# Optimization experiments

Hardware: AMD Instinct MI355X
Metric: run time of the kernel (lower is better)

Reference implementation:

```python
import jax, jax.numpy as jnp
import numpy as np
from jax import lax


def _c1x1(t, w, b=None):
    # t: [B,C,H,W], w: [O,C] (1x1 conv == channel matmul)
    y = jnp.einsum('bchw,oc->bohw', t, w)
    if b is not None:
        y = y + b[None, :, None, None]
    return y


def _mamba(u, in_w, conv_w, conv_b, xproj_w, dt_w, dt_b, A_log, Dp, out_w):
    # u: [B,L,d_model]; Mamba block (mamba_ssm defaults: in/out/x_proj bias=False)
    B, L, _ = u.shape
    d_inner = conv_w.shape[0]
    d_state = A_log.shape[1]
    dt_rank = dt_w.shape[1]
    d_conv = conv_w.shape[2]
    xz = jnp.einsum('bld,ed->ble', u, in_w)          # [B,L,2*d_inner]
    xc, z = xz[..., :d_inner], xz[..., d_inner:]
    # depthwise causal conv1d over seq
    xt = jnp.pad(xc.transpose(0, 2, 1), ((0, 0), (0, 0), (d_conv - 1, 0)))
    xt = lax.conv_general_dilated(xt, conv_w, (1,), 'VALID',
                                  feature_group_count=d_inner,
                                  dimension_numbers=('NCH', 'OIH', 'NCH'))
    xc = jax.nn.silu(xt + conv_b[None, :, None]).transpose(0, 2, 1)  # [B,L,d_inner]
    dbc = jnp.einsum('bld,ed->ble', xc, xproj_w)     # [B,L,dt_rank+2*d_state]
    dt = dbc[..., :dt_rank]
    B_ = dbc[..., dt_rank:dt_rank + d_state]
    C_ = dbc[..., dt_rank + d_state:]
    delta = jax.nn.softplus(jnp.einsum('blr,dr->bld', dt, dt_w) + dt_b)  # [B,L,d_inner]
    A = -jnp.exp(A_log)                              # [d_inner,d_state]
    dA = jnp.exp(delta[..., None] * A)               # [B,L,D,N]
    dBu = delta[..., None] * B_[:, :, None, :] * xc[..., None]
    def step(h, inp):
        dA_t, dBu_t, c_t = inp
        h = dA_t * h + dBu_t                         # [B,D,N]
        y = jnp.einsum('bdn,bn->bd', h, c_t)
        return h, y
    h0 = jnp.zeros((B, d_inner, d_state), dtype=u.dtype)
    _, ys = lax.scan(step, h0, (dA.transpose(1, 0, 2, 3),
                                dBu.transpose(1, 0, 2, 3),
                                C_.transpose(1, 0, 2)))
    y = ys.transpose(1, 0, 2) + xc * Dp              # [B,L,d_inner]
    y = y * jax.nn.silu(z)
    return jnp.einsum('bld,od->blo', y, out_w)       # [B,L,d_model]


def setup_inputs() -> dict:
    key = jax.random.key(0)
    B, C, H, W = 8, 128, 160, 160
    mip, d_in, d_st, d_r, d_cv = 8, 256, 16, 8, 4
    ks = iter(jax.random.split(key, 64))
    def rn(shape, s=0.05):
        return (jax.random.normal(next(ks), shape, dtype=jnp.float32) * s)
    inp = {'x': jax.random.normal(next(ks), (B, C, H, W), dtype=jnp.float32)}
    inp.update(conv1_w=rn((mip, C)), conv1_b=rn((mip,)),
               bn_g=jnp.ones((mip,)), bn_b=jnp.zeros((mip,)),
               bn_m=jnp.zeros((mip,)), bn_v=jnp.ones((mip,)),
               convh_w=rn((C, mip)), convh_b=rn((C,)),
               convw_w=rn((C, mip)), convw_b=rn((C,)),
               mlpx_w1=rn((C, C)), mlpx_b1=rn((C,)), mlpx_w2=rn((C, C)), mlpx_b2=rn((C,)),
               mlpy_w1=rn((C, C)), mlpy_b1=rn((C,)), mlpy_w2=rn((C, C)), mlpy_b2=rn((C,)),
               adjust_w=rn((C, 2 * C)))
    for p in ('mx', 'my'):
        inp[p + '_in_w'] = rn((2 * d_in, C))
        inp[p + '_conv_w'] = rn((d_in, 1, d_cv), 0.3)
        inp[p + '_conv_b'] = rn((d_in,))
        inp[p + '_xproj_w'] = rn((d_r + 2 * d_st, d_in))
        inp[p + '_dt_w'] = rn((d_in, d_r))
        inp[p + '_dt_b'] = rn((d_in,))
        inp[p + '_Alog'] = jnp.log(jnp.broadcast_to(jnp.arange(1, d_st + 1, dtype=jnp.float32), (d_in, d_st)))
        inp[p + '_D'] = jnp.ones((d_in,))
        inp[p + '_out_w'] = rn((C, d_in))
    return inp


def reference(x, conv1_w, conv1_b, bn_g, bn_b, bn_m, bn_v, convh_w, convh_b,
              convw_w, convw_b, mlpx_w1, mlpx_b1, mlpx_w2, mlpx_b2,
              mlpy_w1, mlpy_b1, mlpy_w2, mlpy_b2, adjust_w,
              mx_in_w, mx_conv_w, mx_conv_b, mx_xproj_w, mx_dt_w, mx_dt_b,
              mx_Alog, mx_D, mx_out_w,
              my_in_w, my_conv_w, my_conv_b, my_xproj_w, my_dt_w, my_dt_b,
              my_Alog, my_D, my_out_w):
    B, C, H, W = x.shape
    gelu = lambda t: jax.nn.gelu(t, approximate=False)
    # CoordAttWithMLP
    x_h = x.mean(3, keepdims=True)                      # [B,C,H,1]
    x_w = x.mean(2, keepdims=True).transpose(0, 1, 3, 2)  # [B,C,W,1]
    y = jnp.concatenate([x_h, x_w], axis=2)             # [B,C,H+W,1]
    y = _c1x1(y, conv1_w, conv1_b)
    y = (y - bn_m[None, :, None, None]) * jax.lax.rsqrt(bn_v + 1e-5)[None, :, None, None]
    y = y * bn_g[None, :, None, None] + bn_b[None, :, None, None]
    y = gelu(y)
    a_h = _c1x1(y[:, :, :H], convh_w, convh_b)          # [B,C,H,1] (pre-sigmoid)
    a_w = _c1x1(y[:, :, H:].transpose(0, 1, 3, 2), convw_w, convw_b)  # [B,C,1,W]
    # EfficientMambaAttention00
    ux = x.mean(3).transpose(0, 2, 1)                   # [B,H,C]
    x_x = _mamba(ux, mx_in_w, mx_conv_w, mx_conv_b, mx_xproj_w,
                 mx_dt_w, mx_dt_b, mx_Alog, mx_D, mx_out_w)
    x_x = x_x.transpose(0, 2, 1)[..., None]             # [B,C,H,1]
    x_x = jax.nn.sigmoid(x_x + a_h)
    x_x = _c1x1(gelu(_c1x1(x_x, mlpx_w1, mlpx_b1)), mlpx_w2, mlpx_b2)
    uy = x.mean(2).transpose(0, 2, 1)                   # [B,W,C]
    x_y = _mamba(uy, my_in_w, my_conv_w, my_conv_b, my_xproj_w,
                 my_dt_w, my_dt_b, my_Alog, my_D, my_out_w)
    x_y = x_y.transpose(0, 2, 1)[:, :, None, :]         # [B,C,1,W]
    x_y = jax.nn.sigmoid(x_y + a_w)
    x_y = _c1x1(gelu(_c1x1(x_y, mlpy_w1, mlpy_b1)), mlpy_w2, mlpy_b2)
    # combine
    result_h = jax.nn.sigmoid(a_h) * x_y                # [B,C,H,W]
    result_w = jax.nn.sigmoid(a_w) * x_x                # [B,C,H,W]
    out1 = _c1x1(jnp.concatenate([result_h, result_w], axis=1), adjust_w)
    return x * out1
```

## Files before the change

kernel.cpp:

```cpp
#include <hip/hip_runtime.h>
#include <hip/hip_bf16.h>
#include <math.h>


typedef __attribute__((ext_vector_type(8))) short short8;
typedef __attribute__((ext_vector_type(4))) float f32x4;

__device__ __forceinline__ float sigm_(float x){ return 1.f/(1.f+__expf(-x)); }
__device__ __forceinline__ float silu_(float x){ return x/(1.f+__expf(-x)); }
__device__ __forceinline__ float gelu_(float x){ return 0.5f*x*(1.f+erff(x*0.7071067811865476f)); }
__device__ __forceinline__ float softplus_(float x){ return (x>20.f)?x:log1pf(__expf(x)); }

__global__ void k_means(const float* __restrict__ x, float* __restrict__ xh, float* __restrict__ xw){
  int bc = blockIdx.x;
  const float* xt = x + (size_t)bc*25600;
  int tid = threadIdx.x, wave = tid>>6, lane = tid&63;
  __shared__ float4 colpart[4][40];
  float csx=0.f, csy=0.f, csz=0.f, csw=0.f;
  for (int i=0;i<40;i++){
    int h = wave*40+i;
    float4 v = make_float4(0.f,0.f,0.f,0.f);
    if (lane<40) v = ((const float4*)(xt + h*160))[lane];
    csx+=v.x; csy+=v.y; csz+=v.z; csw+=v.w;
    float r = v.x+v.y+v.z+v.w;
    for (int off=32; off>0; off>>=1) r += __shfl_down(r, off, 64);
    if (lane==0) xh[(size_t)bc*160+h] = r*(1.f/160.f);
  }
  if (lane<40) colpart[wave][lane] = make_float4(csx,csy,csz,csw);
  __syncthreads();
  if (tid<40){
    float4 a=colpart[0][tid], b=colpart[1][tid], c=colpart[2][tid], d=colpart[3][tid];
    float4 s = make_float4((a.x+b.x+c.x+d.x)*(1.f/160.f), (a.y+b.y+c.y+d.y)*(1.f/160.f),
                           (a.z+b.z+c.z+d.z)*(1.f/160.f), (a.w+b.w+c.w+d.w)*(1.f/160.f));
    ((float4*)(xw + (size_t)bc*160))[tid] = s;
  }
}

__global__ void k_ybranch(const float* __restrict__ xh, const float* __restrict__ xw,
                          const float* __restrict__ w1, const float* __restrict__ b1,
                          const float* __restrict__ bg, const float* __restrict__ bb,
                          const float* __restrict__ bm, const float* __restrict__ bv,
                          float* __restrict__ ybuf){
  int gid = blockIdx.x*blockDim.x + threadIdx.x;
  if (gid >= 8*320) return;
  int b = gid/320, p = gid%320;
  const float* in = (p<160) ? (xh + (size_t)b*128*160 + p) : (xw + (size_t)b*128*160 + (p-160));
  float acc[8] = {0,0,0,0,0,0,0,0};
  for (int c=0;c<128;c++){
    float u = in[c*160];
    #pragma unroll
    for (int m=0;m<8;m++) acc[m] += w1[m*128+c]*u;
  }
  #pragma unroll
  for (int m=0;m<8;m++){
    float val = acc[m] + b1[m];
    val = (val - bm[m]) * rsqrtf(bv[m] + 1e-5f);
    val = val * bg[m] + bb[m];
    ybuf[(b*320+p)*8+m] = gelu_(val);
  }
}

__global__ void k_ahw(const float* __restrict__ ybuf,
                      const float* __restrict__ wh, const float* __restrict__ bh,
                      const float* __restrict__ ww, const float* __restrict__ bw,
                      float* __restrict__ a_h, float* __restrict__ a_w,
                      float* __restrict__ SH, float* __restrict__ SW){
  int gid = blockIdx.x*blockDim.x + threadIdx.x;
  if (gid >= 8*128*320) return;
  int p = gid%320; int c = (gid/320)%128; int b = gid/(320*128);
  const float* yv = ybuf + (size_t)(b*320+p)*8;
  const float* w = (p<160)? (wh + c*8) : (ww + c*8);
  float acc = (p<160)? bh[c] : bw[c];
  #pragma unroll
  for (int m=0;m<8;m++) acc += w[m]*yv[m];
  if (p<160){
    size_t o = ((size_t)(b*128+c))*160+p;
    a_h[o] = acc; SH[o] = sigm_(acc);
  } else {
    size_t o = ((size_t)(b*128+c))*160+(p-160);
    a_w[o] = acc; SW[o] = sigm_(acc);
  }
}

__global__ __launch_bounds__(256) void k_inproj(
                         const float* __restrict__ xh, const float* __restrict__ xw,
                         const float* __restrict__ inw0, const float* __restrict__ inw1,
                         float* __restrict__ xcpre, float* __restrict__ zb){
  __shared__ float uS[8][128];
  int blk = blockIdx.x;
  int g = blk/160, rem = blk%160, b = rem/20, lt = rem%20, lbase = lt*8;
  int t = threadIdx.x;
  const float* src = (g==0)? xh : xw;
  {
    int c = t>>1, lh = t&1;
    float4 v = *(const float4*)(src + ((size_t)(b*128+c))*160 + lbase + lh*4);
    uS[lh*4+0][c]=v.x; uS[lh*4+1][c]=v.y; uS[lh*4+2][c]=v.z; uS[lh*4+3][c]=v.w;
  }
  __syncthreads();
  const float* inw = (g==0)? inw0 : inw1;
  const float* w0p = inw + (size_t)t*128;
  const float* w1p = inw + (size_t)(t+256)*128;
  float acc0[8]={0,0,0,0,0,0,0,0}, acc1[8]={0,0,0,0,0,0,0,0};
  for (int ct=0; ct<16; ct++){
    float4 wa = *(const float4*)(w0p + ct*8);
    float4 wb = *(const float4*)(w0p + ct*8 + 4);
    float4 wc = *(const float4*)(w1p + ct*8);
    float4 wd = *(const float4*)(w1p + ct*8 + 4);
    #pragma unroll
    for (int l=0;l<8;l++){
      float4 ua = *(const float4*)&uS[l][ct*8];
      float4 ub = *(const float4*)&uS[l][ct*8+4];
      acc0[l] += wa.x*ua.x + wa.y*ua.y + wa.z*ua.z + wa.w*ua.w
               + wb.x*ub.x + wb.y*ub.y + wb.z*ub.z + wb.w*ub.w;
      acc1[l] += wc.x*ua.x + wc.y*ua.y + wc.z*ua.z + wc.w*ua.w
               + wd.x*ub.x + wd.y*ub.y + wd.z*ub.z + wd.w*ub.w;
    }
  }
  size_t ob = ((size_t)(g*8+b)*160 + lbase)*256;
  #pragma unroll
  for (int l=0;l<8;l++){
    xcpre[ob + (size_t)l*256 + t] = acc0[l];
    zb   [ob + (size_t)l*256 + t] = acc1[l];
  }
}

__global__ void k_conv(const float* __restrict__ xcpre,
                       const float* __restrict__ cw0, const float* __restrict__ cb0,
                       const float* __restrict__ cw1, const float* __restrict__ cb1,
                       float* __restrict__ xcb){
  int gid = blockIdx.x*blockDim.x + threadIdx.x;
  if (gid >= 2*8*160*256) return;
  int d = gid & 255; int t = gid >> 8; int l = t % 160; int gb = t / 160; int g = gb >> 3;
  const float* cw = ((g==0)? cw0 : cw1) + d*4;
  float acc = ((g==0)? cb0 : cb1)[d];
  const float* base = xcpre + (size_t)gb*160*256 + d;
  #pragma unroll
  for (int k=0;k<4;k++){
    int ls = l-3+k;
    if (ls>=0) acc += cw[k] * base[(size_t)ls*256];
  }
  xcb[gid] = silu_(acc);
}

__global__ void k_prep(const float* __restrict__ adjw, __hip_bfloat16* __restrict__ adjwb){
  int i = blockIdx.x*256 + threadIdx.x;
  if (i < 32768) adjwb[i] = __float2bfloat16(adjw[i]);
}

__global__ __launch_bounds__(256) void k_xproj(
                        const float* __restrict__ xcb,
                        const float* __restrict__ xp0, const float* __restrict__ xp1,
                        float* __restrict__ dbc){
  __shared__ float xv[32][260];
  int blk = blockIdx.x;
  int g = blk/40, rem = blk%40, b = rem/5, lt = rem%5, lbase = lt*32;
  int t = threadIdx.x;
  size_t base = ((size_t)(g*8+b)*160 + lbase)*256;
  for (int i=t; i<8192; i+=256){ int l=i>>8, d=i&255; xv[l][d] = xcb[base+i]; }
  __syncthreads();
  int l = t>>3, s = t&7;
  const float* xp = (g==0)? xp0 : xp1;
  size_t orow = ((size_t)(g*8+b)*160 + lbase + l)*40;
  for (int q=0;q<5;q++){
    int j = s + q*8;
    const float* w = xp + j*256;
    float acc=0.f;
    for (int dd=0; dd<256; dd+=8){
      float4 wa = *(const float4*)(w+dd);
      float4 wb = *(const float4*)(w+dd+4);
      float4 ua = *(const float4*)&xv[l][dd];
      float4 ub = *(const float4*)&xv[l][dd+4];
      acc += wa.x*ua.x + wa.y*ua.y + wa.z*ua.z + wa.w*ua.w
           + wb.x*ub.x + wb.y*ub.y + wb.z*ub.z + wb.w*ub.w;
    }
    dbc[orow + j] = acc;
  }
}

__global__ __launch_bounds__(256) void k_scan(
                       const float* __restrict__ dbc,
                       const float* __restrict__ xcb, const float* __restrict__ zb,
                       const float* __restrict__ dtw0, const float* __restrict__ dtb0,
                       const float* __restrict__ dtw1, const float* __restrict__ dtb1,
                       const float* __restrict__ Alog0, const float* __restrict__ Alog1,
                       const float* __restrict__ D0, const float* __restrict__ D1,
                       float* __restrict__ ysb){
  __shared__ float dsS[160][16];
  __shared__ float BS [160][16];
  __shared__ float CS [160][16];
  __shared__ float xcS[160][16];
  __shared__ float yS [160][16];
  int blk = blockIdx.x;
  int gb = blk >> 4, dblk = blk & 15, g = gb >> 3;
  int dbase = dblk*16;
  int t = threadIdx.x;
  size_t base = (size_t)gb*160*256;
  const float* db = dbc + (size_t)gb*6400;
  const float* dtwG = (g==0)? dtw0 : dtw1;
  const float* dtbG = (g==0)? dtb0 : dtb1;

  #pragma unroll
  for (int i=0;i<10;i++){
    int item = t + 256*i;
    int l = item>>4, c = item&15;
    const float* r = db + l*40;
    int d = dbase + c;
    const float* wt = dtwG + d*8;
    float4 w0 = *(const float4*)wt;
    float4 w1 = *(const float4*)(wt+4);
    float4 r0 = *(const float4*)r;
    float4 r1 = *(const float4*)(r+4);
    float dt = dtbG[d] + w0.x*r0.x+w0.y*r0.y+w0.z*r0.z+w0.w*r0.w
                       + w1.x*r1.x+w1.y*r1.y+w1.z*r1.z+w1.w*r1.w;
    dsS[l][c] = softplus_(dt);
    BS [l][c] = r[8+c];
    CS [l][c] = r[24+c];
    xcS[l][c] = xcb[base + (size_t)l*256 + dbase + c];
  }
  __syncthreads();

  int dloc = t>>4, n = t&15;
  int d = dbase + dloc;
  float A  = -__expf(((g==0)? Alog0 : Alog1)[d*16+n]);
  float Dd = ((g==0)? D0 : D1)[d];
  float h = 0.f;
  for (int lc=0; lc<160; lc+=8){
    float ds8[8], B8[8], C8[8], xc8[8];
    #pragma unroll
    for (int j=0;j<8;j++){
      ds8[j]=dsS[lc+j][dloc]; B8[j]=BS[lc+j][n];
      C8[j]=CS[lc+j][n];      xc8[j]=xcS[lc+j][dloc];
    }
    #pragma unroll
    for (int j=0;j<8;j++){
      float dA = __expf(ds8[j]*A);
      h = dA*h + ds8[j]*B8[j]*xc8[j];
      float p = h*C8[j];
      p += __shfl_xor(p,1,16); p += __shfl_xor(p,2,16);
      p += __shfl_xor(p,4,16); p += __shfl_xor(p,8,16);
      if (n==0) yS[lc+j][dloc] = p + xc8[j]*Dd;
    }
  }
  __syncthreads();

  #pragma unroll
  for (int i=0;i<10;i++){
    int item = t + 256*i;
    int l = item>>4, c = item&15;
    size_t gi = base + (size_t)l*256 + dbase + c;
    ysb[gi] = yS[l][c] * silu_(zb[gi]);
  }
}

__global__ __launch_bounds__(256) void k_post(
                       const float* __restrict__ ysb,
                       const float* __restrict__ ow0, const float* __restrict__ ow1,
                       const float* __restrict__ a_h, const float* __restrict__ a_w,
                       const float* __restrict__ w1x, const float* __restrict__ b1x,
                       const float* __restrict__ w1y, const float* __restrict__ b1y,
                       const float* __restrict__ w2x, const float* __restrict__ b2x,
                       const float* __restrict__ w2y, const float* __restrict__ b2y,
                       float* __restrict__ Qx, float* __restrict__ Qy){
  __shared__ float ysS[10][256];
  __shared__ float Sc[10][128];
  __shared__ float Sp[10][128];
  int blk = blockIdx.x;
  int g = blk>>7, rem = blk&127, b = rem>>4, lt = rem&15, lbase = lt*10;
  int t = threadIdx.x; int c = t&127, kh = t>>7;
  size_t ybase = ((size_t)(g*8+b)*160 + lbase)*256;
  for (int i=t; i<2560; i+=256) ((float*)ysS)[i] = ysb[ybase+i];
  __syncthreads();
  float acc[10];
  {
    const float* w = ((g==0)? ow0 : ow1) + (size_t)c*256 + kh*128;
    #pragma unroll
    for (int l=0;l<10;l++) acc[l]=0.f;
    for (int ct=0; ct<16; ct++){
      float4 wa = *(const float4*)(w + ct*8);
      float4 wb = *(const float4*)(w + ct*8 + 4);
      #pragma unroll
      for (int l=0;l<10;l++){
        float4 ua = *(const float4*)&ysS[l][kh*128+ct*8];
        float4 ub = *(const float4*)&ysS[l][kh*128+ct*8+4];
        acc[l] += wa.x*ua.x + wa.y*ua.y + wa.z*ua.z + wa.w*ua.w
                + wb.x*ub.x + wb.y*ub.y + wb.z*ub.z + wb.w*ub.w;
      }
    }
  }
  if (kh==1){ for (int l=0;l<10;l++) Sc[l][c] = acc[l]; }
  __syncthreads();
  if (kh==0){
    const float* a = ((g==0)? a_h : a_w) + ((size_t)(b*128+c))*160 + lbase;
    #pragma unroll
    for (int l=0;l<10;l++) Sp[l][c] = sigm_(acc[l] + Sc[l][c] + a[l]);
  }
  __syncthreads();
  {
    const float* w = ((g==0)? w1x : w1y) + (size_t)c*128 + kh*64;
    #pragma unroll
    for (int l=0;l<10;l++) acc[l]=0.f;
    for (int ct=0; ct<8; ct++){
      float4 wa = *(const float4*)(w + ct*8);
      float4 wb = *(const float4*)(w + ct*8 + 4);
      #pragma unroll
      for (int l=0;l<10;l++){
        float4 ua = *(const float4*)&Sp[l][kh*64+ct*8];
        float4 ub = *(const float4*)&Sp[l][kh*64+ct*8+4];
        acc[l] += wa.x*ua.x + wa.y*ua.y + wa.z*ua.z + wa.w*ua.w
                + wb.x*ub.x + wb.y*ub.y + wb.z*ub.z + wb.w*ub.w;
      }
    }
  }
  if (kh==1){ for (int l=0;l<10;l++) Sc[l][c] = acc[l]; }
  __syncthreads();
  if (kh==0){
    float bb = ((g==0)? b1x : b1y)[c];
    float tv[10];
    #pragma unroll
    for (int l=0;l<10;l++) tv[l] = gelu_(bb + acc[l] + Sc[l][c]);
    __syncthreads();
    #pragma unroll
    for (int l=0;l<10;l++) Sp[l][c] = tv[l];
  } else {
    __syncthreads();
  }
  __syncthreads();
  {
    const float* w = ((g==0)? w2x : w2y) + (size_t)c*128 + kh*64;
    #pragma unroll
    for (int l=0;l<10;l++) acc[l]=0.f;
    for (int ct=0; ct<8; ct++){
      float4 wa = *(const float4*)(w + ct*8);
      float4 wb = *(const float4*)(w + ct*8 + 4);
      #pragma unroll
      for (int l=0;l<10;l++){
        float4 ua = *(const float4*)&Sp[l][kh*64+ct*8];
        float4 ub = *(const float4*)&Sp[l][kh*64+ct*8+4];
        acc[l] += wa.x*ua.x + wa.y*ua.y + wa.z*ua.z + wa.w*ua.w
                + wb.x*ub.x + wb.y*ub.y + wb.z*ub.z + wb.w*ub.w;
      }
    }
  }
  if (kh==1){ for (int l=0;l<10;l++) Sc[l][c] = acc[l]; }
  __syncthreads();
  if (kh==0){
    float bb = ((g==0)? b2x : b2y)[c];
    float* Q = (g==0)? Qx : Qy;
    size_t orow = ((size_t)(b*128+c))*160 + lbase;
    #pragma unroll
    for (int l=0;l<10;l++) Q[orow + l] = bb + acc[l] + Sc[l][c];
  }
}

__global__ __launch_bounds__(256) void k_final_mfma(
                       const float* __restrict__ x,
                       const float* __restrict__ SH, const float* __restrict__ SW,
                       const float* __restrict__ Qx, const float* __restrict__ Qy,
                       const __hip_bfloat16* __restrict__ adjwb, float* __restrict__ out){
  __shared__ __hip_bfloat16 F[80*136];
  int blk = blockIdx.x;
  int b = blk/320; int rem = blk%320; int h = rem>>1; int wh = rem&1;
  int wbase = wh*80;
  int tid = threadIdx.x;
  int kq = tid & 127, whh = tid >> 7;
  int wid = tid>>6, lane = tid&63, quad = lane>>4, l16 = lane&15;

  f32x4 acc[2][5];
  #pragma unroll
  for (int i=0;i<2;i++)
    #pragma unroll
    for (int nt=0;nt<5;nt++) acc[i][nt] = (f32x4){0.f,0.f,0.f,0.f};

  #pragma unroll
  for (int ch=0; ch<2; ch++){
    {
      size_t rowoff = ((size_t)(b*128+kq))*160;
      float s;
      const float* rp;
      if (ch==0){ s = SH[rowoff + h]; rp = Qy + rowoff + wbase + whh*40; }
      else      { s = Qx[rowoff + h]; rp = SW + rowoff + wbase + whh*40; }
      const float4* rp4 = (const float4*)rp;
      #pragma unroll
      for (int u=0; u<10; u++){
        float4 v = rp4[u];
        int wr = whh*40 + u*4;
        F[(wr+0)*136 + kq] = __float2bfloat16(s*v.x);
        F[(wr+1)*136 + kq] = __float2bfloat16(s*v.y);
        F[(wr+2)*136 + kq] = __float2bfloat16(s*v.z);
        F[(wr+3)*136 + kq] = __float2bfloat16(s*v.w);
      }
    }
    __syncthreads();
    short8 bfrag[2][4];
    #pragma unroll
    for (int i=0;i<2;i++){
      const __hip_bfloat16* bp = adjwb + (size_t)((wid*2+i)*16 + l16)*256 + ch*128 + quad*8;
      #pragma unroll
      for (int kc=0;kc<4;kc++) bfrag[i][kc] = *(const short8*)(bp + kc*32);
    }
    #pragma unroll
    for (int nt=0; nt<5; nt++){
      const __hip_bfloat16* ap = &F[(nt*16 + l16)*136 + quad*8];
      #pragma unroll
      for (int kc=0;kc<4;kc++){
        short8 af = *(const short8*)(ap + kc*32);
        acc[0][nt] = __builtin_amdgcn_mfma_f32_16x16x32_bf16(af, bfrag[0][kc], acc[0][nt], 0,0,0);
        acc[1][nt] = __builtin_amdgcn_mfma_f32_16x16x32_bf16(af, bfrag[1][kc], acc[1][nt], 0,0,0);
      }
    }
    if (ch==0) __syncthreads();
  }
  #pragma unroll
  for (int i=0;i<2;i++){
    int o = (wid*2+i)*16 + l16;
    size_t rowb = (((size_t)(b*128+o))*160 + h)*160;
    #pragma unroll
    for (int nt=0; nt<5; nt++){
      int w0 = wbase + nt*16 + quad*4;
      float4 xv = *(const float4*)(x + rowb + w0);
      f32x4 a = acc[i][nt];
      float4 ov = make_float4(xv.x*a[0], xv.y*a[1], xv.z*a[2], xv.w*a[3]);
      *(float4*)(out + rowb + w0) = ov;
    }
  }
}

extern "C" void kernel_launch(void* const* d_in, const int* in_sizes, int n_in,
                              void* d_out, int out_size, void* d_ws, size_t ws_size,
                              hipStream_t stream) {
  #define W(i) ((const float*)d_in[i])
  const float* X = W(0);
  float* ws = (float*)d_ws;
  float* xh    = ws;
  float* xw    = xh    + 163840;
  float* ybuf  = xw    + 163840;
  float* ah    = ybuf  + 20480;
  float* aw    = ah    + 163840;
  float* xcpre = aw    + 163840;
  float* zb    = xcpre + 655360;
  float* xcb   = zb    + 655360;
  float* dbc   = xcb   + 655360;
  float* ysb   = dbc   + 102400;
  float* Qx    = ysb   + 655360;
  float* Qy    = Qx    + 163840;
  __hip_bfloat16* adjwb = (__hip_bfloat16*)xcpre;
  float* SH    = xcpre + 16384;
  float* SW    = SH    + 163840;

  k_means  <<<1024, 256, 0, stream>>>(X, xh, xw);
  k_ybranch<<<10,   256, 0, stream>>>(xh, xw, W(1), W(2), W(3), W(4), W(5), W(6), ybuf);
  k_inproj <<<320,  256, 0, stream>>>(xh, xw, W(20), W(29), xcpre, zb);
  k_conv   <<<2560, 256, 0, stream>>>(xcpre, W(21), W(22), W(30), W(31), xcb);
  k_prep   <<<128,  256, 0, stream>>>(W(19), adjwb);
  k_ahw    <<<1280, 256, 0, stream>>>(ybuf, W(7), W(8), W(9), W(10), ah, aw, SH, SW);
  k_xproj  <<<80,   256, 0, stream>>>(xcb, W(23), W(32), dbc);
  k_scan   <<<256,  256, 0, stream>>>(dbc, xcb, zb, W(24), W(25), W(33), W(34),
                                      W(26), W(35), W(27), W(36), ysb);
  k_post   <<<256,  256, 0, stream>>>(ysb, W(28), W(37), ah, aw,
                                      W(11), W(12), W(15), W(16),
                                      W(13), W(14), W(17), W(18), Qx, Qy);
  k_final_mfma<<<2560, 256, 0, stream>>>(X, SH, SW, Qx, Qy, adjwb, (float*)d_out);
  #undef W
}
```

Baseline: 466.9 us.

## Transpose SH/Qx layouts, prefetch loads, remap blocks and use nontemporal stores in final kernel

SH and Qx are now written transposed ([b,h,c]), so the per-channel scalar loads in the final kernel become coalesced across kq. The final kernel issues all Qy/SW row loads and the x tile loads early, so they overlap the first MFMA phase. The block index is swizzled across batches, and output stores use nontemporal hints to avoid cache pollution. Costs: more registers held live and uncoalesced transposed writes in k_ahw and k_post.

```diff
diff --git a/kernel.cpp b/kernel.cpp
--- a/kernel.cpp
+++ b/kernel.cpp
@@ -64,7 +64,7 @@
                       const float* __restrict__ wh, const float* __restrict__ bh,
                       const float* __restrict__ ww, const float* __restrict__ bw,
                       float* __restrict__ a_h, float* __restrict__ a_w,
-                      float* __restrict__ SH, float* __restrict__ SW){
+                      float* __restrict__ SHT, float* __restrict__ SW){
   int gid = blockIdx.x*blockDim.x + threadIdx.x;
   if (gid >= 8*128*320) return;
   int p = gid%320; int c = (gid/320)%128; int b = gid/(320*128);
@@ -75,7 +75,8 @@
   for (int m=0;m<8;m++) acc += w[m]*yv[m];
   if (p<160){
     size_t o = ((size_t)(b*128+c))*160+p;
-    a_h[o] = acc; SH[o] = sigm_(acc);
+    a_h[o] = acc;
+    SHT[((size_t)(b*160+p))*128 + c] = sigm_(acc);
   } else {
     size_t o = ((size_t)(b*128+c))*160+(p-160);
     a_w[o] = acc; SW[o] = sigm_(acc);
@@ -260,7 +261,7 @@
                        const float* __restrict__ w1y, const float* __restrict__ b1y,
                        const float* __restrict__ w2x, const float* __restrict__ b2x,
                        const float* __restrict__ w2y, const float* __restrict__ b2y,
-                       float* __restrict__ Qx, float* __restrict__ Qy){
+                       float* __restrict__ QxT, float* __restrict__ Qy){
   __shared__ float ysS[10][256];
   __shared__ float Sc[10][128];
   __shared__ float Sp[10][128];
@@ -345,56 +346,65 @@
   __syncthreads();
   if (kh==0){
     float bb = ((g==0)? b2x : b2y)[c];
-    float* Q = (g==0)? Qx : Qy;
-    size_t orow = ((size_t)(b*128+c))*160 + lbase;
-    #pragma unroll
-    for (int l=0;l<10;l++) Q[orow + l] = bb + acc[l] + Sc[l][c];
+    if (g==0){
+      #pragma unroll
+      for (int l=0;l<10;l++)
+        QxT[((size_t)(b*160 + lbase + l))*128 + c] = bb + acc[l] + Sc[l][c];
+    } else {
+      size_t orow = ((size_t)(b*128+c))*160 + lbase;
+      #pragma unroll
+      for (int l=0;l<10;l++) Qy[orow + l] = bb + acc[l] + Sc[l][c];
+    }
   }
 }
 
 __global__ __launch_bounds__(256) void k_final_mfma(
                        const float* __restrict__ x,
-                       const float* __restrict__ SH, const float* __restrict__ SW,
-                       const float* __restrict__ Qx, const float* __restrict__ Qy,
+                       const float* __restrict__ SHT, const float* __restrict__ SW,
+                       const float* __restrict__ QxT, const float* __restrict__ Qy,
                        const __hip_bfloat16* __restrict__ adjwb, float* __restrict__ out){
   __shared__ __hip_bfloat16 F[80*136];
-  int blk = blockIdx.x;
+  int blk0 = blockIdx.x;
+  int blk = (blk0 & 7)*320 + (blk0 >> 3);
   int b = blk/320; int rem = blk%320; int h = rem>>1; int wh = rem&1;
   int wbase = wh*80;
   int tid = threadIdx.x;
   int kq = tid & 127, whh = tid >> 7;
   int wid = tid>>6, lane = tid&63, quad = lane>>4, l16 = lane&15;
 
+  float s0 = SHT[((size_t)(b*160+h))*128 + kq];
+  float s1 = QxT[((size_t)(b*160+h))*128 + kq];
+
+  size_t prow = ((size_t)(b*128+kq))*160 + wbase + whh*40;
+  const float4* rp0 = (const float4*)(Qy + prow);
+  const float4* rp1 = (const float4*)(SW + prow);
+
+  float4 v0[10], v1[10];
+  #pragma unroll
+  for (int u=0;u<10;u++) v0[u] = rp0[u];
+  #pragma unroll
+  for (int u=0;u<10;u++) v1[u] = rp1[u];
+  #pragma unroll
+  for (int u=0;u<10;u++){
+    int wr = whh*40 + u*4;
+    F[(wr+0)*136 + kq] = __float2bfloat16(s0*v0[u].x);
+    F[(wr+1)*136 + kq] = __float2bfloat16(s0*v0[u].y);
+    F[(wr+2)*136 + kq] = __float2bfloat16(s0*v0[u].z);
+    F[(wr+3)*136 + kq] = __float2bfloat16(s0*v0[u].w);
+  }
+  __syncthreads();
+
   f32x4 acc[2][5];
   #pragma unroll
   for (int i=0;i<2;i++)
     #pragma unroll
     for (int nt=0;nt<5;nt++) acc[i][nt] = (f32x4){0.f,0.f,0.f,0.f};
 
-  #pragma unroll
-  for (int ch=0; ch<2; ch++){
-    {
-      size_t rowoff = ((size_t)(b*128+kq))*160;
-      float s;
-      const float* rp;
-      if (ch==0){ s = SH[rowoff + h]; rp = Qy + rowoff + wbase + whh*40; }
-      else      { s = Qx[rowoff + h]; rp = SW + rowoff + wbase + whh*40; }
-      const float4* rp4 = (const float4*)rp;
-      #pragma unroll
-      for (int u=0; u<10; u++){
-        float4 v = rp4[u];
-        int wr = whh*40 + u*4;
-        F[(wr+0)*136 + kq] = __float2bfloat16(s*v.x);
-        F[(wr+1)*136 + kq] = __float2bfloat16(s*v.y);
-        F[(wr+2)*136 + kq] = __float2bfloat16(s*v.z);
-        F[(wr+3)*136 + kq] = __float2bfloat16(s*v.w);
-      }
-    }
-    __syncthreads();
+  {
     short8 bfrag[2][4];
     #pragma unroll
     for (int i=0;i<2;i++){
-      const __hip_bfloat16* bp = adjwb + (size_t)((wid*2+i)*16 + l16)*256 + ch*128 + quad*8;
+      const __hip_bfloat16* bp = adjwb + (size_t)((wid*2+i)*16 + l16)*256 + quad*8;
       #pragma unroll
       for (int kc=0;kc<4;kc++) bfrag[i][kc] = *(const short8*)(bp + kc*32);
     }
@@ -408,19 +418,56 @@
         acc[1][nt] = __builtin_amdgcn_mfma_f32_16x16x32_bf16(af, bfrag[1][kc], acc[1][nt], 0,0,0);
       }
     }
-    if (ch==0) __syncthreads();
-  }
+  }
+  __syncthreads();
+
+  #pragma unroll
+  for (int u=0;u<10;u++){
+    int wr = whh*40 + u*4;
+    F[(wr+0)*136 + kq] = __float2bfloat16(s1*v1[u].x);
+    F[(wr+1)*136 + kq] = __float2bfloat16(s1*v1[u].y);
+    F[(wr+2)*136 + kq] = __float2bfloat16(s1*v1[u].z);
+    F[(wr+3)*136 + kq] = __float2bfloat16(s1*v1[u].w);
+  }
+  float4 xv[2][5];
+  size_t rbA = (((size_t)(b*128 + (wid*2+0)*16 + l16))*160 + h)*160 + wbase + quad*4;
+  size_t rbB = (((size_t)(b*128 + (wid*2+1)*16 + l16))*160 + h)*160 + wbase + quad*4;
+  #pragma unroll
+  for (int nt=0;nt<5;nt++){
+    xv[0][nt] = *(const float4*)(x + rbA + nt*16);
+    xv[1][nt] = *(const float4*)(x + rbB + nt*16);
+  }
+  __syncthreads();
+
+  {
+    short8 bfrag[2][4];
+    #pragma unroll
+    for (int i=0;i<2;i++){
+      const __hip_bfloat16* bp = adjwb + (size_t)((wid*2+i)*16 + l16)*256 + 128 + quad*8;
+      #pragma unroll
+      for (int kc=0;kc<4;kc++) bfrag[i][kc] = *(const short8*)(bp + kc*32);
+    }
+    #pragma unroll
+    for (int nt=0; nt<5; nt++){
+      const __hip_bfloat16* ap = &F[(nt*16 + l16)*136 + quad*8];
+      #pragma unroll
+      for (int kc=0;kc<4;kc++){
+        short8 af = *(const short8*)(ap + kc*32);
+        acc[0][nt] = __builtin_amdgcn_mfma_f32_16x16x32_bf16(af, bfrag[0][kc], acc[0][nt], 0,0,0);
+        acc[1][nt] = __builtin_amdgcn_mfma_f32_16x16x32_bf16(af, bfrag[1][kc], acc[1][nt], 0,0,0);
+      }
+    }
+  }
+
   #pragma unroll
   for (int i=0;i<2;i++){
-    int o = (wid*2+i)*16 + l16;
-    size_t rowb = (((size_t)(b*128+o))*160 + h)*160;
+    size_t rb = i? rbB : rbA;
     #pragma unroll
     for (int nt=0; nt<5; nt++){
-      int w0 = wbase + nt*16 + quad*4;
-      float4 xv = *(const float4*)(x + rowb + w0);
       f32x4 a = acc[i][nt];
-      float4 ov = make_float4(xv.x*a[0], xv.y*a[1], xv.z*a[2], xv.w*a[3]);
-      *(float4*)(out + rowb + w0) = ov;
+      float4 xvv = xv[i][nt];
+      f32x4 ov = (f32x4){xvv.x*a[0], xvv.y*a[1], xvv.z*a[2], xvv.w*a[3]};
+      __builtin_nontemporal_store(ov, (f32x4*)(out + rb + nt*16));
     }
   }
 }
@@ -441,24 +488,24 @@
   float* xcb   = zb    + 655360;
   float* dbc   = xcb   + 655360;
   float* ysb   = dbc   + 102400;
-  float* Qx    = ysb   + 655360;
-  float* Qy    = Qx    + 163840;
+  float* QxT   = ysb   + 655360;
+  float* Qy    = QxT   + 163840;
   __hip_bfloat16* adjwb = (__hip_bfloat16*)xcpre;
-  float* SH    = xcpre + 16384;
-  float* SW    = SH    + 163840;
+  float* SHT   = xcpre + 16384;
+  float* SW    = SHT   + 163840;
 
   k_means  <<<1024, 256, 0, stream>>>(X, xh, xw);
   k_ybranch<<<10,   256, 0, stream>>>(xh, xw, W(1), W(2), W(3), W(4), W(5), W(6), ybuf);
   k_inproj <<<320,  256, 0, stream>>>(xh, xw, W(20), W(29), xcpre, zb);
   k_conv   <<<2560, 256, 0, stream>>>(xcpre, W(21), W(22), W(30), W(31), xcb);
   k_prep   <<<128,  256, 0, stream>>>(W(19), adjwb);
-  k_ahw    <<<1280, 256, 0, stream>>>(ybuf, W(7), W(8), W(9), W(10), ah, aw, SH, SW);
+  k_ahw    <<<1280, 256, 0, stream>>>(ybuf, W(7), W(8), W(9), W(10), ah, aw, SHT, SW);
   k_xproj  <<<80,   256, 0, stream>>>(xcb, W(23), W(32), dbc);
   k_scan   <<<256,  256, 0, stream>>>(dbc, xcb, zb, W(24), W(25), W(33), W(34),
                                       W(26), W(35), W(27), W(36), ysb);
   k_post   <<<256,  256, 0, stream>>>(ysb, W(28), W(37), ah, aw,
                                       W(11), W(12), W(15), W(16),
-                                      W(13), W(14), W(17), W(18), Qx, Qy);
-  k_final_mfma<<<2560, 256, 0, stream>>>(X, SH, SW, Qx, Qy, adjwb, (float*)d_out);
+                                      W(13), W(14), W(17), W(18), QxT, Qy);
+  k_final_mfma<<<2560, 256, 0, stream>>>(X, SHT, SW, QxT, Qy, adjwb, (float*)d_out);
   #undef W
 }
```

Result: no change. 458.2 us (-1.9%).
